# Kernel tuning notes

Measured on AMD Instinct MI355X. Metric: run time of the kernel, lower is better.

Reference implementation:

```python
import jax, jax.numpy as jnp
import numpy as np
from jax import lax

EPS = 1e-5

def setup_inputs() -> dict:
    key = jax.random.key(0)
    ks = jax.random.split(key, 8)
    B, D, H, W = 2, 96, 96, 96
    K, N, R = 4, 16, 6
    return {
        "x": jax.random.normal(ks[0], (B, D, H, W), jnp.float32),
        "x_proj_weight": jax.random.normal(ks[1], (K, R + 2 * N, D), jnp.float32) * 0.05,
        "dt_projs_weight": jax.random.normal(ks[2], (K, D, R), jnp.float32) * 0.05,
        "dt_projs_bias": jax.random.normal(ks[3], (K, D), jnp.float32) * 0.05,
        "A_logs": jax.random.uniform(ks[4], (K * D, N), jnp.float32, 0.0, 1.0),
        "Ds": jax.random.normal(ks[5], (K * D,), jnp.float32) * 0.1,
        "norm_weight": jnp.ones((D,), jnp.float32),
        "norm_bias": jnp.zeros((D,), jnp.float32),
    }

def _cross_scan(x):
    # x: [B,C,H,W] -> xs: [B,4,C,L]; dirs: row-major, col-major, and their flips
    B, C, H, W = x.shape
    x_hw = x.reshape(B, C, H * W)
    x_wh = jnp.swapaxes(x, 2, 3).reshape(B, C, H * W)
    return jnp.stack([x_hw, x_wh, x_hw[..., ::-1], x_wh[..., ::-1]], axis=1)

def _cross_merge(ys, H, W):
    # ys: [B,4,C,L] -> y: [B,C,L]
    B, K, C, L = ys.shape
    ys = ys[:, 0:2] + ys[:, 2:4][..., ::-1]
    y_wh = jnp.swapaxes(ys[:, 1].reshape(B, C, W, H), 2, 3).reshape(B, C, L)
    return ys[:, 0] + y_wh

def _forward(x, x_proj_weight, dt_projs_weight, dt_projs_bias, A_logs, Ds,
             norm_weight, norm_bias):
    B, D, H, W = x.shape
    L = H * W
    K, _, R = dt_projs_weight.shape
    N = A_logs.shape[1]

    xs = _cross_scan(x)                                        # [B,K,D,L]
    x_dbl = jnp.einsum('bkdl,kcd->bkcl', xs, x_proj_weight)    # [B,K,R+2N,L]
    dts, Bs, Cs = x_dbl[:, :, :R], x_dbl[:, :, R:R + N], x_dbl[:, :, R + N:]
    dts = jnp.einsum('bkrl,kdr->bkdl', dts, dt_projs_weight)   # [B,K,D,L]

    A = -jnp.exp(A_logs).reshape(K, D, N)                      # [K,D,N]
    delta = jax.nn.softplus(dts + dt_projs_bias[None, :, :, None])  # [B,K,D,L]

    # time-major for scan
    u_t = jnp.moveaxis(xs, 3, 0)       # [L,B,K,D]
    d_t = jnp.moveaxis(delta, 3, 0)    # [L,B,K,D]
    B_t = jnp.moveaxis(Bs, 3, 0)       # [L,B,K,N]
    C_t = jnp.moveaxis(Cs, 3, 0)       # [L,B,K,N]

    def step(h, inp):
        u, dlt, b, c = inp
        h = jnp.exp(dlt[..., None] * A) * h + (dlt * u)[..., None] * b[:, :, None, :]
        y = jnp.einsum('bkdn,bkn->bkd', h, c)
        return h, y

    h0 = jnp.zeros((B, K, D, N), xs.dtype)
    _, ys = lax.scan(step, h0, (u_t, d_t, B_t, C_t))           # ys: [L,B,K,D]
    ys = jnp.moveaxis(ys, 0, 3)                                # [B,K,D,L]
    ys = ys + Ds.reshape(1, K, D, 1) * xs                      # skip term

    y = _cross_merge(ys, H, W)                                 # [B,D,L]
    y = jnp.swapaxes(y, 1, 2)                                  # [B,L,D]
    # out_norm: LayerNorm over channel dim
    mu = y.mean(-1, keepdims=True)
    var = y.var(-1, keepdims=True)
    y = (y - mu) / jnp.sqrt(var + EPS) * norm_weight + norm_bias
    return y.reshape(B, H, W, D)

def reference(x, x_proj_weight, dt_projs_weight, dt_projs_bias, A_logs, Ds,
              norm_weight, norm_bias):
    return _forward(x, x_proj_weight, dt_projs_weight, dt_projs_bias,
                    A_logs, Ds, norm_weight, norm_bias)
```

## Files before the change

### kernel.cpp

```cpp
#include <hip/hip_runtime.h>
#include <hip/hip_bf16.h>
#include <hip/hip_fp16.h>


constexpr int Bn = 2, Kn = 4, Dn = 96, Hn = 96, Wn = 96, Ln = Hn * Wn;
constexpr int Nn = 16, Rn = 6;
constexpr int CCn = 144, CLn = 64;

#define DI __device__ __forceinline__

typedef _Float16 half2v __attribute__((ext_vector_type(2)));

DI float bf2f(unsigned short u) { return __uint_as_float(((unsigned)u) << 16); }
DI bool probe_bf16(const void* nw) { return ((const unsigned*)nw)[0] == 0x3F803F80u; }
DI float ld_in(const void* p, long i, bool bf) {
  return bf ? bf2f(((const unsigned short*)p)[i]) : ((const float*)p)[i];
}
DI float fexp2(float x) {
#if __has_builtin(__builtin_amdgcn_exp2f)
  return __builtin_amdgcn_exp2f(x);
#else
  return exp2f(x);
#endif
}
DI float softplus_fast(float v) {
  return (v > 15.f) ? v : __logf(1.f + __expf(v));
}
DI float dot2acc(unsigned a, unsigned b, float c) {
#if __has_builtin(__builtin_amdgcn_fdot2)
  half2v av, bv;
  __builtin_memcpy(&av, &a, 4);
  __builtin_memcpy(&bv, &b, 4);
  return __builtin_amdgcn_fdot2(av, bv, c, false);
#else
  __half2 ah = *(__half2*)&a, bh = *(__half2*)&b;
  float2 af = __half22float2(ah), bf2_ = __half22float2(bh);
  return fmaf(af.y, bf2_.y, fmaf(af.x, bf2_.x, c));
#endif
}
DI float quad_reduce_add(float v) {
  int a = __builtin_amdgcn_mov_dpp(__float_as_int(v), 0xB1, 0xF, 0xF, true);
  v += __int_as_float(a);
  int b = __builtin_amdgcn_mov_dpp(__float_as_int(v), 0x4E, 0xF, 0xF, true);
  v += __int_as_float(b);
  return v;
}
constexpr float LOG2E = 1.44269504088896340736f;

__global__ __launch_bounds__(256) void k_prep(
    const void* __restrict__ x, const void* __restrict__ xpw,
    const void* __restrict__ dtw, const void* __restrict__ dtb,
    const void* __restrict__ Al, const void* __restrict__ Ds,
    const void* __restrict__ nw, const void* __restrict__ nb,
    float* __restrict__ xl, float* __restrict__ xlT,
    float* __restrict__ wp_f, float* __restrict__ wdt_f,
    float* __restrict__ bias_f, float* __restrict__ Al_f,
    float* __restrict__ dsum, float* __restrict__ nw_f, float* __restrict__ nb_f) {
  __shared__ float tile[96 * 97];
  bool bf = probe_bf16(nw);
  int h = blockIdx.x, b = blockIdx.y;
  int tid = threadIdx.x;
  int fi = (blockIdx.y * gridDim.x + blockIdx.x) * 256 + tid;
  int fgs = gridDim.x * gridDim.y * 256;
  for (int i = fi; i < Kn * 38 * Dn; i += fgs) wp_f[i] = ld_in(xpw, i, bf);
  for (int i = fi; i < Kn * Dn * Rn; i += fgs) wdt_f[i] = ld_in(dtw, i, bf);
  for (int i = fi; i < Kn * Dn; i += fgs) bias_f[i] = ld_in(dtb, i, bf);
  for (int i = fi; i < Kn * Dn * Nn; i += fgs)
    Al_f[i] = -__expf(ld_in(Al, i, bf)) * LOG2E;
  for (int i = fi; i < Dn; i += fgs) {
    dsum[i] = ld_in(Ds, i, bf) + ld_in(Ds, 96 + i, bf) +
              ld_in(Ds, 192 + i, bf) + ld_in(Ds, 288 + i, bf);
    nw_f[i] = ld_in(nw, i, bf);
    nb_f[i] = ld_in(nb, i, bf);
  }
  long srcbase = (long)b * Dn * Ln + (long)h * 96;
  for (int i = tid; i < 96 * 96; i += 256) {
    int d = i / 96, w = i - d * 96;
    tile[d * 97 + w] = ld_in(x, srcbase + (long)d * Ln + w, bf);
  }
  __syncthreads();
  float* xlb = xl + (size_t)b * Ln * 96;
  float* xTb = xlT + (size_t)b * Ln * 96;
  for (int i = tid; i < 96 * 96; i += 256) {
    int w = i / 96, d = i - w * 96;
    float v = tile[d * 97 + w];
    xlb[(size_t)(h * 96 + w) * 96 + d] = v;
    xTb[(size_t)(w * 96 + h) * 96 + d] = v;
  }
}

__global__ __launch_bounds__(256) void k_proj(
    const float* __restrict__ xl, const float* __restrict__ xlT,
    const float* __restrict__ wp_f, const float* __restrict__ wdt_f,
    const float* __restrict__ bias_f,
    __half2* __restrict__ ddu, __half* __restrict__ BCh) {
  constexpr int TL = 64;
  __shared__ __half xt[TL * 102];
  __shared__ __half wp[40 * 100];
  __shared__ __half xd[40 * 72];
  __shared__ float wdt[96 * 6];
  __shared__ float bias[96];
  int tile = blockIdx.x, k = blockIdx.y, b = blockIdx.z;
  int l0 = tile * TL;
  int tid = threadIdx.x;
  bool rev = (k & 2) != 0;

  for (int i = tid; i < 40 * 100; i += 256) {
    int c = i / 100, dd = i - c * 100;
    wp[i] = __float2half((c < 38 && dd < 96) ? wp_f[k * 38 * 96 + c * 96 + dd]
                                             : 0.f);
  }
  for (int i = tid; i < 96 * 6; i += 256) wdt[i] = wdt_f[k * 96 * 6 + i];
  if (tid < 96) bias[tid] = bias_f[k * 96 + tid];
  {
    const float* xsrc = ((k & 1) ? xlT : xl) + (size_t)b * Ln * 96;
    for (int i = tid; i < TL * 24; i += 256) {
      int r = i / 24, q = i - r * 24;
      int g = rev ? (Ln - 1 - l0 - r) : (l0 + r);
      float4 v = *(const float4*)(xsrc + (size_t)g * 96 + q * 4);
      *(__half2*)(&xt[r * 102 + q * 4]) = __floats2half2_rn(v.x, v.y);
      *(__half2*)(&xt[r * 102 + q * 4 + 2]) = __floats2half2_rn(v.z, v.w);
    }
  }
  __syncthreads();

  {
    int jg = tid & 31, cg = tid >> 5;
    int j0 = jg * 2, c0 = cg * 5;
    float acc[5][2];
#pragma unroll
    for (int i = 0; i < 5; ++i) { acc[i][0] = 0.f; acc[i][1] = 0.f; }
    for (int dd = 0; dd < 96; dd += 4) {
      uint2 xa = *(const uint2*)&xt[(j0 + 0) * 102 + dd];
      uint2 xb = *(const uint2*)&xt[(j0 + 1) * 102 + dd];
#pragma unroll
      for (int i = 0; i < 5; ++i) {
        uint2 wv = *(const uint2*)&wp[(c0 + i) * 100 + dd];
        acc[i][0] = dot2acc(xa.x, wv.x, acc[i][0]);
        acc[i][0] = dot2acc(xa.y, wv.y, acc[i][0]);
        acc[i][1] = dot2acc(xb.x, wv.x, acc[i][1]);
        acc[i][1] = dot2acc(xb.y, wv.y, acc[i][1]);
      }
    }
#pragma unroll
    for (int i = 0; i < 5; ++i)
      *(__half2*)&xd[(c0 + i) * 72 + j0] = __floats2half2_rn(acc[i][0], acc[i][1]);
  }
  __syncthreads();

  size_t bk = (size_t)b * 4 + k;
  {
    __half2* o = (__half2*)(BCh + (bk * (size_t)Ln + l0) * 32);
    for (int i = tid; i < TL * 16; i += 256) {
      int j = i >> 4, cp = i & 15;
      int c = cp * 2;
      int ng = c >> 3, idx = c & 7;
      int ch = (idx < 4) ? (6 + ng * 4 + idx) : (22 + ng * 4 + (idx - 4));
      o[i] = __halves2half2(xd[ch * 72 + j], xd[(ch + 1) * 72 + j]);
    }
  }
  {
    int lp = tid >> 2, q = tid & 3, d0 = q * 24;
    float xr[6];
#pragma unroll
    for (int r = 0; r < 6; ++r) xr[r] = __half2float(xd[r * 72 + lp]);
    __half2* orow = ddu + (bk * (size_t)Ln + l0 + lp) * 96 + d0;
#pragma unroll
    for (int ii = 0; ii < 6; ++ii) {
      union { uint4 u4; __half2 h2[4]; } pk;
#pragma unroll
      for (int p = 0; p < 4; ++p) {
        int d = d0 + ii * 4 + p;
        float v = bias[d];
#pragma unroll
        for (int r = 0; r < 6; ++r) v = fmaf(xr[r], wdt[d * 6 + r], v);
        float sp = softplus_fast(v);
        float u = __half2float(xt[lp * 102 + d]);
        pk.h2[p] = __floats2half2_rn(sp, sp * u);
      }
      *(uint4*)(orow + ii * 4) = pk.u4;
    }
  }
}

__global__ __launch_bounds__(384) void k_scan1(
    const __half2* __restrict__ ddu, const __half* __restrict__ BCh,
    const float* __restrict__ Al_f, float* __restrict__ PSg) {
  __shared__ __half2 dd_s[CLn * 96];
  __shared__ float b_s[CLn * 16];
  int chunk = blockIdx.x, k = blockIdx.y, b = blockIdx.z;
  int tid = threadIdx.x;
  int d = tid >> 2, ng = tid & 3, n0 = ng * 4;
  int bk = b * 4 + k;
  int bkd = bk * 96 + d;
  int t0 = chunk * CLn;
  float ac[4];
#pragma unroll
  for (int j = 0; j < 4; ++j) ac[j] = Al_f[(k * 96 + d) * 16 + n0 + j];
  {
    const uint4* dsrc = (const uint4*)(ddu + ((size_t)bk * Ln + t0) * 96);
    uint4* ddst = (uint4*)dd_s;
    for (int i = tid; i < CLn * 96 / 4; i += 384) ddst[i] = dsrc[i];
    const uint2* bsrc = (const uint2*)(BCh + ((size_t)bk * Ln + t0) * 32);
    for (int i = tid; i < CLn * 4; i += 384) {
      int t = i >> 2, g = i & 3;
      union { uint2 u; __half2 h2[2]; } raw;
      raw.u = bsrc[t * 8 + g * 2];
      float2 f01 = __half22float2(raw.h2[0]);
      float2 f23 = __half22float2(raw.h2[1]);
      *(float4*)&b_s[t * 16 + g * 4] = make_float4(f01.x, f01.y, f23.x, f23.y);
    }
  }
  __syncthreads();

  float P[4] = {1.f, 1.f, 1.f, 1.f}, S[4] = {0.f, 0.f, 0.f, 0.f};
#pragma unroll 4
  for (int t = 0; t < CLn; ++t) {
    float2 f = __half22float2(dd_s[t * 96 + d]);
    float4 Bv = *(const float4*)&b_s[t * 16 + n0];
    const float* Ba = (const float*)&Bv;
#pragma unroll
    for (int j = 0; j < 4; ++j) {
      float a = fexp2(f.x * ac[j]);
      P[j] *= a;
      S[j] = fmaf(a, S[j], f.y * Ba[j]);
    }
  }
  size_t ob = ((size_t)bkd * CCn + chunk) * 32 + n0;
  *(float4*)(PSg + ob) = make_float4(P[0], P[1], P[2], P[3]);
  *(float4*)(PSg + ob + 16) = make_float4(S[0], S[1], S[2], S[3]);
}

__global__ __launch_bounds__(256) void k_midscan(float* __restrict__ PSg) {
  __shared__ float Pl[256], Sl[256];
  int bkd = blockIdx.x;
  int tid = threadIdx.x;
  int g = tid >> 4, n = tid & 15;
  constexpr int CPG = CCn / 16;
  size_t base = ((size_t)bkd * CCn + (size_t)g * CPG) * 32 + n;
  float Pr[CPG], Sr[CPG];
#pragma unroll
  for (int i = 0; i < CPG; ++i) {
    Pr[i] = PSg[base + (size_t)i * 32];
    Sr[i] = PSg[base + (size_t)i * 32 + 16];
  }
  float Pa = 1.f, Sa = 0.f;
#pragma unroll
  for (int i = 0; i < CPG; ++i) { Sa = fmaf(Pr[i], Sa, Sr[i]); Pa *= Pr[i]; }
  Pl[tid] = Pa;
  Sl[tid] = Sa;
  __syncthreads();
#pragma unroll
  for (int s = 1; s < 16; s <<= 1) {
    float Pp = 1.f, Sp = 0.f;
    if (g >= s) { Pp = Pl[(g - s) * 16 + n]; Sp = Sl[(g - s) * 16 + n]; }
    __syncthreads();
    if (g >= s) {
      Sl[tid] = fmaf(Pl[tid], Sp, Sl[tid]);
      Pl[tid] *= Pp;
    }
    __syncthreads();
  }
  float h = (g == 0) ? 0.f : Sl[(g - 1) * 16 + n];
#pragma unroll
  for (int i = 0; i < CPG; ++i) {
    PSg[base + (size_t)i * 32] = h;
    h = fmaf(Pr[i], h, Sr[i]);
  }
}

__global__ __launch_bounds__(384) void k_scan2(
    const __half2* __restrict__ ddu, const __half* __restrict__ BCh,
    const float* __restrict__ Al_f, const float* __restrict__ PSg,
    __half* __restrict__ ysH) {
  __shared__ __half2 dd_s[CLn * 96];
  __shared__ __half bc_s[CLn * 32];
  int chunk = blockIdx.x, k = blockIdx.y, b = blockIdx.z;
  int tid = threadIdx.x;
  int d = tid >> 2, ng = tid & 3, n0 = ng * 4;
  int bk = b * 4 + k;
  int bkd = bk * 96 + d;
  int t0 = chunk * CLn;
  float ac[4];
#pragma unroll
  for (int j = 0; j < 4; ++j) ac[j] = Al_f[(k * 96 + d) * 16 + n0 + j];
  {
    const uint4* dsrc = (const uint4*)(ddu + ((size_t)bk * Ln + t0) * 96);
    uint4* ddst = (uint4*)dd_s;
    for (int i = tid; i < CLn * 96 / 4; i += 384) ddst[i] = dsrc[i];
    const uint4* bsrc = (const uint4*)(BCh + ((size_t)bk * Ln + t0) * 32);
    uint4* bdst = (uint4*)bc_s;
    for (int i = tid; i < CLn * 32 * 2 / 16; i += 384) bdst[i] = bsrc[i];
  }
  float4 h4 = *(const float4*)(PSg + ((size_t)bkd * CCn + chunk) * 32 + n0);
  float h[4] = {h4.x, h4.y, h4.z, h4.w};
  __syncthreads();

#pragma unroll 4
  for (int t = 0; t < CLn; ++t) {
    float2 f = __half22float2(dd_s[t * 96 + d]);
    union { uint4 u; __half2 h2[4]; } bc;
    bc.u = *(const uint4*)&bc_s[t * 32 + ng * 8];
    float2 b01 = __half22float2(bc.h2[0]);
    float2 b23 = __half22float2(bc.h2[1]);
    float2 c01 = __half22float2(bc.h2[2]);
    float2 c23 = __half22float2(bc.h2[3]);
    float Ba[4] = {b01.x, b01.y, b23.x, b23.y};
    float Ca[4] = {c01.x, c01.y, c23.x, c23.y};
    float py = 0.f;
#pragma unroll
    for (int j = 0; j < 4; ++j) {
      float a = fexp2(f.x * ac[j]);
      h[j] = fmaf(a, h[j], f.y * Ba[j]);
      py = fmaf(h[j], Ca[j], py);
    }
    py = quad_reduce_add(py);
    if (ng == 0) ysH[((size_t)bk * Ln + t0 + t) * 96 + d] = __float2half(py);
  }
}

__global__ __launch_bounds__(256) void k_merge_ln(
    const __half* __restrict__ ysH, const float* __restrict__ xl,
    const float* __restrict__ dsum, const void* __restrict__ nwraw,
    const float* __restrict__ nw_f, const float* __restrict__ nb_f,
    void* __restrict__ outv) {
  __shared__ float yt[64 * 97];
  __shared__ float nwf[96], nbf[96], mu_s[64], rs_s[64];
  bool bf = probe_bf16(nwraw);
  int tile = blockIdx.x, b = blockIdx.y;
  int h0 = (tile / 12) * 8, w0 = (tile % 12) * 8;
  int tid = threadIdx.x;
  if (tid < 96) { nwf[tid] = nw_f[tid]; nbf[tid] = nb_f[tid]; }
  const __half* y0 = ysH + (size_t)(b * 4 + 0) * Ln * 96;
  const __half* y1 = ysH + (size_t)(b * 4 + 1) * Ln * 96;
  const __half* y2 = ysH + (size_t)(b * 4 + 2) * Ln * 96;
  const __half* y3 = ysH + (size_t)(b * 4 + 3) * Ln * 96;
  const float* xb = xl + (size_t)b * Ln * 96;
  for (int i = tid; i < 64 * 96; i += 256) {
    int rr = i / 96, d = i - rr * 96;
    int hh = h0 + (rr >> 3), ww = w0 + (rr & 7);
    int l = hh * 96 + ww, t1 = ww * 96 + hh;
    float v = __half2float(y0[(size_t)l * 96 + d]) +
              __half2float(y1[(size_t)t1 * 96 + d]) +
              __half2float(y2[(size_t)(Ln - 1 - l) * 96 + d]) +
              __half2float(y3[(size_t)(Ln - 1 - t1) * 96 + d]) +
              dsum[d] * xb[(size_t)l * 96 + d];
    yt[rr * 97 + d] = v;
  }
  __syncthreads();
  if (tid < 64) {
    float s = 0.f, ss = 0.f;
#pragma unroll 4
    for (int d = 0; d < 96; ++d) {
      float v = yt[tid * 97 + d];
      s += v;
      ss += v * v;
    }
    float mu = s * (1.f / 96.f);
    float var = fmaxf(ss * (1.f / 96.f) - mu * mu, 0.f);
    mu_s[tid] = mu;
    rs_s[tid] = rsqrtf(var + 1e-5f);
  }
  __syncthreads();
  for (int i = tid; i < 64 * 96; i += 256) {
    int rr = i / 96, d = i - rr * 96;
    int hh = h0 + (rr >> 3), ww = w0 + (rr & 7);
    size_t idx = ((size_t)b * Ln + hh * 96 + ww) * 96 + d;
    float v = (yt[rr * 97 + d] - mu_s[rr]) * rs_s[rr] * nwf[d] + nbf[d];
    if (bf) ((__hip_bfloat16*)outv)[idx] = __float2bfloat16(v);
    else    ((float*)outv)[idx] = v;
  }
}

extern "C" void kernel_launch(void* const* d_in, const int* in_sizes, int n_in,
                              void* d_out, int out_size, void* d_ws, size_t ws_size,
                              hipStream_t stream) {
  const void* x   = d_in[0];
  const void* xpw = d_in[1];
  const void* dtw = d_in[2];
  const void* dtb = d_in[3];
  const void* Al  = d_in[4];
  const void* Ds  = d_in[5];
  const void* nw  = d_in[6];
  const void* nb  = d_in[7];

  char* ws = (char*)d_ws;
  size_t off = 0;
  auto alloc = [&](size_t bytes) {
    char* p = ws + off;
    off += (bytes + 511) & ~(size_t)511;
    return p;
  };
  float* xl    = (float*)alloc((size_t)Bn * Ln * Dn * 4);
  float* xlT   = (float*)alloc((size_t)Bn * Ln * Dn * 4);
  float* wp_f  = (float*)alloc((size_t)Kn * 38 * Dn * 4);
  float* wdt_f = (float*)alloc((size_t)Kn * Dn * Rn * 4);
  float* bias_f= (float*)alloc((size_t)Kn * Dn * 4);
  float* Al_f  = (float*)alloc((size_t)Kn * Dn * Nn * 4);
  float* dsum  = (float*)alloc((size_t)Dn * 4);
  float* nw_f  = (float*)alloc((size_t)Dn * 4);
  float* nb_f  = (float*)alloc((size_t)Dn * 4);
  __half2* ddu = (__half2*)alloc((size_t)Bn * Kn * Ln * Dn * 4);
  __half* BCh  = (__half*)alloc((size_t)Bn * Kn * Ln * 32 * 2);
  float* PS    = (float*)alloc((size_t)Bn * Kn * Dn * CCn * 32 * 4);
  __half* ysH  = (__half*)alloc((size_t)Bn * Kn * Ln * Dn * 2);
  (void)ws_size; (void)in_sizes; (void)n_in; (void)out_size;

  k_prep<<<dim3(Hn, Bn), dim3(256), 0, stream>>>(
      x, xpw, dtw, dtb, Al, Ds, nw, nb, xl, xlT, wp_f, wdt_f, bias_f, Al_f,
      dsum, nw_f, nb_f);
  k_proj<<<dim3(Ln / 64, Kn, Bn), dim3(256), 0, stream>>>(xl, xlT, wp_f, wdt_f,
                                                          bias_f, ddu, BCh);
  k_scan1<<<dim3(CCn, Kn, Bn), dim3(384), 0, stream>>>(ddu, BCh, Al_f, PS);
  k_midscan<<<dim3(Bn * Kn * Dn), dim3(256), 0, stream>>>(PS);
  k_scan2<<<dim3(CCn, Kn, Bn), dim3(384), 0, stream>>>(ddu, BCh, Al_f, PS, ysH);
  k_merge_ln<<<dim3(144, Bn), dim3(256), 0, stream>>>(ysH, xl, dsum, nw, nw_f,
                                                      nb_f, d_out);
}
```

Measured before the change: 195.9 us.

## Process two channels per thread in scans and vectorize projection and merge kernels

Both scan kernels now assign two channels per thread with 192-thread blocks, so each shared-memory B/C load is reused across two channels and the y outputs are written as half2. The projection kernel transposes the intermediate x_dbl tile to row-major and computes the dt projection with packed fp16 dot products, using fp16 weights. The merge/LayerNorm kernel is vectorized to two channels per thread and spreads the row statistics across four threads with a quad reduction. Halving the thread count per scan block lowers parallelism per block, and fp16 dt weights add a little rounding error.

```diff
diff --git a/kernel.cpp b/kernel.cpp
--- a/kernel.cpp
+++ b/kernel.cpp
@@ -97,8 +97,8 @@
   constexpr int TL = 64;
   __shared__ __half xt[TL * 102];
   __shared__ __half wp[40 * 100];
-  __shared__ __half xd[40 * 72];
-  __shared__ float wdt[96 * 6];
+  __shared__ __half xd2[TL * 40];
+  __shared__ unsigned wdt_u[96 * 4];
   __shared__ float bias[96];
   int tile = blockIdx.x, k = blockIdx.y, b = blockIdx.z;
   int l0 = tile * TL;
@@ -110,7 +110,12 @@
     wp[i] = __float2half((c < 38 && dd < 96) ? wp_f[k * 38 * 96 + c * 96 + dd]
                                              : 0.f);
   }
-  for (int i = tid; i < 96 * 6; i += 256) wdt[i] = wdt_f[k * 96 * 6 + i];
+  for (int i = tid; i < 96 * 3; i += 256) {
+    int d = i / 3, rr = i - d * 3;
+    __half2 hv = __floats2half2_rn(wdt_f[k * 576 + d * 6 + rr * 2],
+                                   wdt_f[k * 576 + d * 6 + rr * 2 + 1]);
+    wdt_u[d * 4 + rr] = *(unsigned*)&hv;
+  }
   if (tid < 96) bias[tid] = bias_f[k * 96 + tid];
   {
     const float* xsrc = ((k & 1) ? xlT : xl) + (size_t)b * Ln * 96;
@@ -143,8 +148,10 @@
       }
     }
 #pragma unroll
-    for (int i = 0; i < 5; ++i)
-      *(__half2*)&xd[(c0 + i) * 72 + j0] = __floats2half2_rn(acc[i][0], acc[i][1]);
+    for (int i = 0; i < 5; ++i) {
+      xd2[j0 * 40 + c0 + i] = __float2half(acc[i][0]);
+      xd2[(j0 + 1) * 40 + c0 + i] = __float2half(acc[i][1]);
+    }
   }
   __syncthreads();
 
@@ -156,79 +163,96 @@
       int c = cp * 2;
       int ng = c >> 3, idx = c & 7;
       int ch = (idx < 4) ? (6 + ng * 4 + idx) : (22 + ng * 4 + (idx - 4));
-      o[i] = __halves2half2(xd[ch * 72 + j], xd[(ch + 1) * 72 + j]);
+      o[i] = *(const __half2*)&xd2[j * 40 + ch];
     }
   }
   {
     int lp = tid >> 2, q = tid & 3, d0 = q * 24;
-    float xr[6];
-#pragma unroll
-    for (int r = 0; r < 6; ++r) xr[r] = __half2float(xd[r * 72 + lp]);
+    uint2 xr01 = *(const uint2*)&xd2[lp * 40];
+    unsigned xr2 = *(const unsigned*)&xd2[lp * 40 + 4];
     __half2* orow = ddu + (bk * (size_t)Ln + l0 + lp) * 96 + d0;
 #pragma unroll
     for (int ii = 0; ii < 6; ++ii) {
       union { uint4 u4; __half2 h2[4]; } pk;
+      __half2 u01 = *(const __half2*)&xt[lp * 102 + d0 + ii * 4];
+      __half2 u23 = *(const __half2*)&xt[lp * 102 + d0 + ii * 4 + 2];
+      float2 uf01 = __half22float2(u01), uf23 = __half22float2(u23);
+      float uv[4] = {uf01.x, uf01.y, uf23.x, uf23.y};
 #pragma unroll
       for (int p = 0; p < 4; ++p) {
         int d = d0 + ii * 4 + p;
-        float v = bias[d];
-#pragma unroll
-        for (int r = 0; r < 6; ++r) v = fmaf(xr[r], wdt[d * 6 + r], v);
+        uint2 wv = *(const uint2*)&wdt_u[d * 4];
+        unsigned wv2 = wdt_u[d * 4 + 2];
+        float v = dot2acc(xr01.x, wv.x,
+                  dot2acc(xr01.y, wv.y,
+                  dot2acc(xr2, wv2, bias[d])));
         float sp = softplus_fast(v);
-        float u = __half2float(xt[lp * 102 + d]);
-        pk.h2[p] = __floats2half2_rn(sp, sp * u);
+        pk.h2[p] = __floats2half2_rn(sp, sp * uv[p]);
       }
       *(uint4*)(orow + ii * 4) = pk.u4;
     }
   }
 }
 
-__global__ __launch_bounds__(384) void k_scan1(
+__global__ __launch_bounds__(192) void k_scan1(
     const __half2* __restrict__ ddu, const __half* __restrict__ BCh,
     const float* __restrict__ Al_f, float* __restrict__ PSg) {
   __shared__ __half2 dd_s[CLn * 96];
-  __shared__ float b_s[CLn * 16];
+  __shared__ __half b_s[CLn * 16];
   int chunk = blockIdx.x, k = blockIdx.y, b = blockIdx.z;
   int tid = threadIdx.x;
-  int d = tid >> 2, ng = tid & 3, n0 = ng * 4;
+  int dp = tid >> 2, ng = tid & 3;
+  int d0 = dp * 2, n0 = ng * 4;
   int bk = b * 4 + k;
-  int bkd = bk * 96 + d;
   int t0 = chunk * CLn;
-  float ac[4];
-#pragma unroll
-  for (int j = 0; j < 4; ++j) ac[j] = Al_f[(k * 96 + d) * 16 + n0 + j];
+  float ac[2][4];
+#pragma unroll
+  for (int dd = 0; dd < 2; ++dd)
+#pragma unroll
+    for (int j = 0; j < 4; ++j)
+      ac[dd][j] = Al_f[(k * 96 + d0 + dd) * 16 + n0 + j];
   {
     const uint4* dsrc = (const uint4*)(ddu + ((size_t)bk * Ln + t0) * 96);
     uint4* ddst = (uint4*)dd_s;
-    for (int i = tid; i < CLn * 96 / 4; i += 384) ddst[i] = dsrc[i];
+    for (int i = tid; i < CLn * 96 / 4; i += 192) ddst[i] = dsrc[i];
     const uint2* bsrc = (const uint2*)(BCh + ((size_t)bk * Ln + t0) * 32);
-    for (int i = tid; i < CLn * 4; i += 384) {
+    uint2* bdst = (uint2*)b_s;
+    for (int i = tid; i < CLn * 4; i += 192) {
       int t = i >> 2, g = i & 3;
-      union { uint2 u; __half2 h2[2]; } raw;
-      raw.u = bsrc[t * 8 + g * 2];
-      float2 f01 = __half22float2(raw.h2[0]);
-      float2 f23 = __half22float2(raw.h2[1]);
-      *(float4*)&b_s[t * 16 + g * 4] = make_float4(f01.x, f01.y, f23.x, f23.y);
-    }
-  }
-  __syncthreads();
-
-  float P[4] = {1.f, 1.f, 1.f, 1.f}, S[4] = {0.f, 0.f, 0.f, 0.f};
-#pragma unroll 4
+      bdst[t * 4 + g] = bsrc[t * 8 + g * 2];
+    }
+  }
+  __syncthreads();
+
+  float P[2][4] = {{1.f, 1.f, 1.f, 1.f}, {1.f, 1.f, 1.f, 1.f}};
+  float S[2][4] = {{0.f, 0.f, 0.f, 0.f}, {0.f, 0.f, 0.f, 0.f}};
+#pragma unroll 2
   for (int t = 0; t < CLn; ++t) {
-    float2 f = __half22float2(dd_s[t * 96 + d]);
-    float4 Bv = *(const float4*)&b_s[t * 16 + n0];
-    const float* Ba = (const float*)&Bv;
+    union { uint2 u; __half2 h2[2]; } dv;
+    dv.u = *(const uint2*)&dd_s[t * 96 + d0];
+    union { uint2 u; __half2 h2[2]; } bv;
+    bv.u = *(const uint2*)&b_s[t * 16 + n0];
+    float2 f0 = __half22float2(dv.h2[0]);
+    float2 f1 = __half22float2(dv.h2[1]);
+    float2 B01 = __half22float2(bv.h2[0]);
+    float2 B23 = __half22float2(bv.h2[1]);
+    float Ba[4] = {B01.x, B01.y, B23.x, B23.y};
 #pragma unroll
     for (int j = 0; j < 4; ++j) {
-      float a = fexp2(f.x * ac[j]);
-      P[j] *= a;
-      S[j] = fmaf(a, S[j], f.y * Ba[j]);
-    }
-  }
-  size_t ob = ((size_t)bkd * CCn + chunk) * 32 + n0;
-  *(float4*)(PSg + ob) = make_float4(P[0], P[1], P[2], P[3]);
-  *(float4*)(PSg + ob + 16) = make_float4(S[0], S[1], S[2], S[3]);
+      float a0 = fexp2(f0.x * ac[0][j]);
+      P[0][j] *= a0;
+      S[0][j] = fmaf(a0, S[0][j], f0.y * Ba[j]);
+      float a1 = fexp2(f1.x * ac[1][j]);
+      P[1][j] *= a1;
+      S[1][j] = fmaf(a1, S[1][j], f1.y * Ba[j]);
+    }
+  }
+  size_t ob0 = ((size_t)(bk * 96 + d0) * CCn + chunk) * 32 + n0;
+  size_t ob1 = ((size_t)(bk * 96 + d0 + 1) * CCn + chunk) * 32 + n0;
+  *(float4*)(PSg + ob0) = make_float4(P[0][0], P[0][1], P[0][2], P[0][3]);
+  *(float4*)(PSg + ob0 + 16) = make_float4(S[0][0], S[0][1], S[0][2], S[0][3]);
+  *(float4*)(PSg + ob1) = make_float4(P[1][0], P[1][1], P[1][2], P[1][3]);
+  *(float4*)(PSg + ob1 + 16) = make_float4(S[1][0], S[1][1], S[1][2], S[1][3]);
 }
 
 __global__ __launch_bounds__(256) void k_midscan(float* __restrict__ PSg) {
@@ -269,7 +293,7 @@
   }
 }
 
-__global__ __launch_bounds__(384) void k_scan2(
+__global__ __launch_bounds__(192) void k_scan2(
     const __half2* __restrict__ ddu, const __half* __restrict__ BCh,
     const float* __restrict__ Al_f, const float* __restrict__ PSg,
     __half* __restrict__ ysH) {
@@ -277,45 +301,58 @@
   __shared__ __half bc_s[CLn * 32];
   int chunk = blockIdx.x, k = blockIdx.y, b = blockIdx.z;
   int tid = threadIdx.x;
-  int d = tid >> 2, ng = tid & 3, n0 = ng * 4;
+  int dp = tid >> 2, ng = tid & 3;
+  int d0 = dp * 2, n0 = ng * 4;
   int bk = b * 4 + k;
-  int bkd = bk * 96 + d;
   int t0 = chunk * CLn;
-  float ac[4];
-#pragma unroll
-  for (int j = 0; j < 4; ++j) ac[j] = Al_f[(k * 96 + d) * 16 + n0 + j];
+  float ac[2][4];
+#pragma unroll
+  for (int dd = 0; dd < 2; ++dd)
+#pragma unroll
+    for (int j = 0; j < 4; ++j)
+      ac[dd][j] = Al_f[(k * 96 + d0 + dd) * 16 + n0 + j];
   {
     const uint4* dsrc = (const uint4*)(ddu + ((size_t)bk * Ln + t0) * 96);
     uint4* ddst = (uint4*)dd_s;
-    for (int i = tid; i < CLn * 96 / 4; i += 384) ddst[i] = dsrc[i];
+    for (int i = tid; i < CLn * 96 / 4; i += 192) ddst[i] = dsrc[i];
     const uint4* bsrc = (const uint4*)(BCh + ((size_t)bk * Ln + t0) * 32);
     uint4* bdst = (uint4*)bc_s;
-    for (int i = tid; i < CLn * 32 * 2 / 16; i += 384) bdst[i] = bsrc[i];
-  }
-  float4 h4 = *(const float4*)(PSg + ((size_t)bkd * CCn + chunk) * 32 + n0);
-  float h[4] = {h4.x, h4.y, h4.z, h4.w};
-  __syncthreads();
-
-#pragma unroll 4
+    for (int i = tid; i < CLn * 32 * 2 / 16; i += 192) bdst[i] = bsrc[i];
+  }
+  float4 ha = *(const float4*)(PSg + ((size_t)(bk * 96 + d0) * CCn + chunk) * 32 + n0);
+  float4 hb = *(const float4*)(PSg + ((size_t)(bk * 96 + d0 + 1) * CCn + chunk) * 32 + n0);
+  float h[2][4] = {{ha.x, ha.y, ha.z, ha.w}, {hb.x, hb.y, hb.z, hb.w}};
+  __syncthreads();
+
+#pragma unroll 2
   for (int t = 0; t < CLn; ++t) {
-    float2 f = __half22float2(dd_s[t * 96 + d]);
+    union { uint2 u; __half2 h2[2]; } dv;
+    dv.u = *(const uint2*)&dd_s[t * 96 + d0];
     union { uint4 u; __half2 h2[4]; } bc;
     bc.u = *(const uint4*)&bc_s[t * 32 + ng * 8];
+    float2 f0 = __half22float2(dv.h2[0]);
+    float2 f1 = __half22float2(dv.h2[1]);
     float2 b01 = __half22float2(bc.h2[0]);
     float2 b23 = __half22float2(bc.h2[1]);
     float2 c01 = __half22float2(bc.h2[2]);
     float2 c23 = __half22float2(bc.h2[3]);
     float Ba[4] = {b01.x, b01.y, b23.x, b23.y};
     float Ca[4] = {c01.x, c01.y, c23.x, c23.y};
-    float py = 0.f;
+    float py0 = 0.f, py1 = 0.f;
 #pragma unroll
     for (int j = 0; j < 4; ++j) {
-      float a = fexp2(f.x * ac[j]);
-      h[j] = fmaf(a, h[j], f.y * Ba[j]);
-      py = fmaf(h[j], Ca[j], py);
-    }
-    py = quad_reduce_add(py);
-    if (ng == 0) ysH[((size_t)bk * Ln + t0 + t) * 96 + d] = __float2half(py);
+      float a0 = fexp2(f0.x * ac[0][j]);
+      h[0][j] = fmaf(a0, h[0][j], f0.y * Ba[j]);
+      py0 = fmaf(h[0][j], Ca[j], py0);
+      float a1 = fexp2(f1.x * ac[1][j]);
+      h[1][j] = fmaf(a1, h[1][j], f1.y * Ba[j]);
+      py1 = fmaf(h[1][j], Ca[j], py1);
+    }
+    py0 = quad_reduce_add(py0);
+    py1 = quad_reduce_add(py1);
+    if (ng == 0)
+      *(__half2*)&ysH[((size_t)bk * Ln + t0 + t) * 96 + d0] =
+          __halves2half2(__float2half(py0), __float2half(py1));
   }
 }
 
@@ -324,51 +361,74 @@
     const float* __restrict__ dsum, const void* __restrict__ nwraw,
     const float* __restrict__ nw_f, const float* __restrict__ nb_f,
     void* __restrict__ outv) {
-  __shared__ float yt[64 * 97];
-  __shared__ float nwf[96], nbf[96], mu_s[64], rs_s[64];
+  __shared__ float yt[64 * 98];
+  __shared__ float nwf[96], nbf[96], dsm[96], mu_s[64], rs_s[64];
   bool bf = probe_bf16(nwraw);
   int tile = blockIdx.x, b = blockIdx.y;
   int h0 = (tile / 12) * 8, w0 = (tile % 12) * 8;
   int tid = threadIdx.x;
-  if (tid < 96) { nwf[tid] = nw_f[tid]; nbf[tid] = nb_f[tid]; }
+  if (tid < 96) {
+    nwf[tid] = nw_f[tid];
+    nbf[tid] = nb_f[tid];
+    dsm[tid] = dsum[tid];
+  }
   const __half* y0 = ysH + (size_t)(b * 4 + 0) * Ln * 96;
   const __half* y1 = ysH + (size_t)(b * 4 + 1) * Ln * 96;
   const __half* y2 = ysH + (size_t)(b * 4 + 2) * Ln * 96;
   const __half* y3 = ysH + (size_t)(b * 4 + 3) * Ln * 96;
   const float* xb = xl + (size_t)b * Ln * 96;
-  for (int i = tid; i < 64 * 96; i += 256) {
-    int rr = i / 96, d = i - rr * 96;
+  __syncthreads();
+  for (int i = tid; i < 64 * 48; i += 256) {
+    int rr = i / 48, dp = i - rr * 48, d = dp * 2;
     int hh = h0 + (rr >> 3), ww = w0 + (rr & 7);
     int l = hh * 96 + ww, t1 = ww * 96 + hh;
-    float v = __half2float(y0[(size_t)l * 96 + d]) +
-              __half2float(y1[(size_t)t1 * 96 + d]) +
-              __half2float(y2[(size_t)(Ln - 1 - l) * 96 + d]) +
-              __half2float(y3[(size_t)(Ln - 1 - t1) * 96 + d]) +
-              dsum[d] * xb[(size_t)l * 96 + d];
-    yt[rr * 97 + d] = v;
-  }
-  __syncthreads();
-  if (tid < 64) {
+    float2 v0 = __half22float2(*(const __half2*)&y0[(size_t)l * 96 + d]);
+    float2 v1 = __half22float2(*(const __half2*)&y1[(size_t)t1 * 96 + d]);
+    float2 v2 = __half22float2(*(const __half2*)&y2[(size_t)(Ln - 1 - l) * 96 + d]);
+    float2 v3 = __half22float2(*(const __half2*)&y3[(size_t)(Ln - 1 - t1) * 96 + d]);
+    float2 xv = *(const float2*)&xb[(size_t)l * 96 + d];
+    float2 r;
+    r.x = v0.x + v1.x + v2.x + v3.x + dsm[d] * xv.x;
+    r.y = v0.y + v1.y + v2.y + v3.y + dsm[d + 1] * xv.y;
+    *(float2*)&yt[rr * 98 + d] = r;
+  }
+  __syncthreads();
+  {
+    int rr = tid >> 2, qq = tid & 3;
     float s = 0.f, ss = 0.f;
 #pragma unroll 4
-    for (int d = 0; d < 96; ++d) {
-      float v = yt[tid * 97 + d];
+    for (int d2 = 0; d2 < 24; ++d2) {
+      float v = yt[rr * 98 + qq * 24 + d2];
       s += v;
       ss += v * v;
     }
-    float mu = s * (1.f / 96.f);
-    float var = fmaxf(ss * (1.f / 96.f) - mu * mu, 0.f);
-    mu_s[tid] = mu;
-    rs_s[tid] = rsqrtf(var + 1e-5f);
-  }
-  __syncthreads();
-  for (int i = tid; i < 64 * 96; i += 256) {
-    int rr = i / 96, d = i - rr * 96;
+    s = quad_reduce_add(s);
+    ss = quad_reduce_add(ss);
+    if (qq == 0) {
+      float mu = s * (1.f / 96.f);
+      float var = fmaxf(ss * (1.f / 96.f) - mu * mu, 0.f);
+      mu_s[rr] = mu;
+      rs_s[rr] = rsqrtf(var + 1e-5f);
+    }
+  }
+  __syncthreads();
+  for (int i = tid; i < 64 * 48; i += 256) {
+    int rr = i / 48, dp = i - rr * 48, d = dp * 2;
     int hh = h0 + (rr >> 3), ww = w0 + (rr & 7);
     size_t idx = ((size_t)b * Ln + hh * 96 + ww) * 96 + d;
-    float v = (yt[rr * 97 + d] - mu_s[rr]) * rs_s[rr] * nwf[d] + nbf[d];
-    if (bf) ((__hip_bfloat16*)outv)[idx] = __float2bfloat16(v);
-    else    ((float*)outv)[idx] = v;
+    float2 yv = *(const float2*)&yt[rr * 98 + d];
+    float mu = mu_s[rr], rs = rs_s[rr];
+    float o0 = (yv.x - mu) * rs * nwf[d] + nbf[d];
+    float o1 = (yv.y - mu) * rs * nwf[d + 1] + nbf[d + 1];
+    if (bf) {
+      union { unsigned u; unsigned short us[2]; } pk;
+      __hip_bfloat16 b0 = __float2bfloat16(o0), b1 = __float2bfloat16(o1);
+      pk.us[0] = *(unsigned short*)&b0;
+      pk.us[1] = *(unsigned short*)&b1;
+      *(unsigned*)&((__hip_bfloat16*)outv)[idx] = pk.u;
+    } else {
+      *(float2*)&((float*)outv)[idx] = make_float2(o0, o1);
+    }
   }
 }
 
@@ -411,9 +471,9 @@
       dsum, nw_f, nb_f);
   k_proj<<<dim3(Ln / 64, Kn, Bn), dim3(256), 0, stream>>>(xl, xlT, wp_f, wdt_f,
                                                           bias_f, ddu, BCh);
-  k_scan1<<<dim3(CCn, Kn, Bn), dim3(384), 0, stream>>>(ddu, BCh, Al_f, PS);
+  k_scan1<<<dim3(CCn, Kn, Bn), dim3(192), 0, stream>>>(ddu, BCh, Al_f, PS);
   k_midscan<<<dim3(Bn * Kn * Dn), dim3(256), 0, stream>>>(PS);
-  k_scan2<<<dim3(CCn, Kn, Bn), dim3(384), 0, stream>>>(ddu, BCh, Al_f, PS, ysH);
+  k_scan2<<<dim3(CCn, Kn, Bn), dim3(192), 0, stream>>>(ddu, BCh, Al_f, PS, ysH);
   k_merge_ln<<<dim3(144, Bn), dim3(256), 0, stream>>>(ysH, xl, dsum, nw, nw_f,
                                                       nb_f, d_out);
 }
```

Result: no change. 196.5 us (+0.3%).
